# Optimization experiments

Measured on AMD Instinct MI355X. Metric: run time of the kernel, lower is better.

## Reference

```python
import jax, jax.numpy as jnp
import numpy as np


def _dct_mat(n):
    # Unnormalized DCT-II (torch_dct norm=None): X_k = 2 * sum_i x_i cos(pi*k*(2i+1)/(2n))
    idx = jnp.arange(n, dtype=jnp.float32)
    k = idx[:, None]
    i = idx[None, :]
    return 2.0 * jnp.cos(jnp.pi * k * (2.0 * i + 1.0) / (2.0 * n))  # [n_freq, n_pos]


def _idct_mat(n):
    # Exact inverse of _dct_mat: x_i = (1/n) * (X_0/2 + sum_{k>=1} X_k cos(pi*k*(2i+1)/(2n)))
    idx = jnp.arange(n, dtype=jnp.float32)
    i = idx[:, None]
    k = idx[None, :]
    w = jnp.where(jnp.arange(n) == 0, 0.5, 1.0) / n  # halve DC term
    return jnp.cos(jnp.pi * k * (2.0 * i + 1.0) / (2.0 * n)) * w[None, :]  # [n_pos, n_freq]


def _dct2(x, DH, DW):
    # separable 2D DCT-II over last two axes
    return jnp.einsum('nchw,kh,lw->nckl', x, DH, DW)


def _idct2(x, MH, MW):
    return jnp.einsum('nckl,hk,wl->nchw', x, MH, MW)


def setup_inputs() -> dict:
    key = jax.random.key(0)
    kx, kw = jax.random.split(key)
    x = jax.random.normal(kx, (64, 256, 32, 32), dtype=jnp.float32)
    # kaiming-uniform-like scale for a 256x3x3 fan-in
    weight = jax.random.normal(kw, (256, 256, 3, 3), dtype=jnp.float32) * 0.02
    return {"x": x, "weight": weight}


def reference(x, weight):
    N, C, H, W = x.shape
    F, _, HH, WW = weight.shape
    # pad filter on bottom/right to the full input spatial size
    kpad = jnp.pad(weight, ((0, 0), (0, 0), (0, H - HH), (0, W - WW)))
    DH, DW = _dct_mat(H), _dct_mat(W)
    MH, MW = _idct_mat(H), _idct_mat(W)
    X = _dct2(x, DH, DW)        # [N,C,H,W] frequency domain
    K = _dct2(kpad, DH, DW)     # [F,C,H,W] frequency domain
    # per-frequency channel contraction: matmul([N,C] x [C,F]) at every (h,w)
    R = jnp.einsum('nchw,fchw->nfhw', X, K)
    out = _idct2(R, MH, MW)
    out_H = H - HH + 1
    out_W = W - WW + 1
    return out[..., :out_H, :out_W]
```

## Files before the change

kernel.cpp:

```cpp
#include <hip/hip_runtime.h>
#include <hip/hip_bf16.h>

typedef __bf16 bf16x8 __attribute__((ext_vector_type(8)));
typedef float  f32x4  __attribute__((ext_vector_type(4)));
typedef unsigned short u16;
typedef u16 ushort8_t __attribute__((ext_vector_type(8)));

#define PI_D 3.14159265358979323846

__device__ __forceinline__ float rfl_f(float x){
  return __builtin_bit_cast(float, __builtin_amdgcn_readfirstlane(__builtin_bit_cast(int, x)));
}
__device__ __forceinline__ u16 bf16_bits(float f){
  __bf16 b = (__bf16)f;
  return __builtin_bit_cast(u16, b);
}
__device__ __forceinline__ float bf2f(u16 u){
  return __builtin_bit_cast(float, ((unsigned)u) << 16);
}

__global__ void k_init(float* __restrict__ Dm, float* __restrict__ Mm){
  for (int idx = threadIdx.x; idx < 1024; idx += 256){
    int r = idx >> 5, c = idx & 31;
    Dm[idx] = (float)(2.0 * cos(PI_D * (double)r * (double)(2*c+1) / 64.0));
    Mm[idx] = (float)(cos(PI_D * (double)c * (double)(2*r+1) / 64.0) * ((c==0)?0.5:1.0) / 32.0);
  }
}

__global__ __launch_bounds__(256) void k_wkb(const float* __restrict__ w,
                                             const float* __restrict__ Dm,
                                             u16* __restrict__ wkb){
  __shared__ float dks[32][3];
  int t = threadIdx.x;
  if (t < 96) dks[t/3][t%3] = Dm[(t/3)*32 + (t%3)];
  __syncthreads();
  int f = blockIdx.x, kf0 = blockIdx.y*4, c = t;
  const float* s = w + ((size_t)f*256 + c)*9;
  float wv9[9];
  #pragma unroll
  for (int j = 0; j < 9; ++j) wv9[j] = s[j];
  #pragma unroll
  for (int kq = 0; kq < 4; ++kq){
    int kf = kf0 + kq;
    float d0 = dks[kf][0], d1 = dks[kf][1], d2 = dks[kf][2];
    #pragma unroll
    for (int b = 0; b < 3; ++b){
      float v = d0*wv9[b] + d1*wv9[3+b] + d2*wv9[6+b];
      wkb[((size_t)(kf*3 + b) << 16) + (f << 8) + c] = bf16_bits(v);
    }
  }
}

__global__ __launch_bounds__(256) void k_dct2(const float* __restrict__ x,
                                              const float* __restrict__ Dm,
                                              u16* __restrict__ Xt){
  __shared__ __bf16 Dmb[32][40];
  __shared__ float  xl[4][32*37];
  __shared__ __bf16 t1[4][32*40];
  __shared__ u16    st[1024][20];
  int t = threadIdx.x;
  for (int idx = t; idx < 1024; idx += 256)
    Dmb[idx>>5][idx&31] = (__bf16)Dm[idx];
  __syncthreads();
  int wv = t >> 6, lane = t & 63, l4 = lane & 15, g = lane >> 4;
  bf16x8 dmf[2];
  dmf[0] = *(const bf16x8*)&Dmb[l4][g*8];
  dmf[1] = *(const bf16x8*)&Dmb[16+l4][g*8];
  int n = blockIdx.x, cb = blockIdx.y * 16;
  float* xw = xl[wv];
  __bf16* tw = t1[wv];
  f32x4 z = {0.f,0.f,0.f,0.f};
  for (int ci = 0; ci < 4; ++ci){
    int cl = wv*4 + ci;
    const float* xs = x + ((size_t)(n*256 + cb + cl)) * 1024;
    #pragma unroll
    for (int jr = 0; jr < 4; ++jr){
      int e = jr*256 + lane*4;
      float4 v = *(const float4*)(xs + e);
      float* p = xw + (e>>5)*37 + (e&31);
      p[0]=v.x; p[1]=v.y; p[2]=v.z; p[3]=v.w;
    }
    bf16x8 bf[2];
    #pragma unroll
    for (int nn = 0; nn < 2; ++nn){
      #pragma unroll
      for (int jj = 0; jj < 8; ++jj)
        bf[nn][jj] = (__bf16)xw[(g*8+jj)*37 + nn*16 + l4];
    }
    #pragma unroll
    for (int m = 0; m < 2; ++m){
      #pragma unroll
      for (int nn = 0; nn < 2; ++nn){
        f32x4 d = __builtin_amdgcn_mfma_f32_16x16x32_bf16(dmf[m], bf[nn], z, 0,0,0);
        #pragma unroll
        for (int r = 0; r < 4; ++r)
          tw[(m*16 + g*4 + r)*40 + nn*16 + l4] = (__bf16)d[r];
      }
    }
    bf16x8 a2[2];
    a2[0] = *(const bf16x8*)&tw[(l4)*40 + g*8];
    a2[1] = *(const bf16x8*)&tw[(16+l4)*40 + g*8];
    #pragma unroll
    for (int m2 = 0; m2 < 2; ++m2){
      #pragma unroll
      for (int nn2 = 0; nn2 < 2; ++nn2){
        f32x4 d = __builtin_amdgcn_mfma_f32_16x16x32_bf16(a2[m2], dmf[nn2], z, 0,0,0);
        #pragma unroll
        for (int r = 0; r < 4; ++r){
          int kk = m2*16 + g*4 + r, ll = nn2*16 + l4;
          st[kk*32 + ll][cl] = bf16_bits(d[r]);
        }
      }
    }
  }
  __syncthreads();
  #pragma unroll
  for (int rr = 0; rr < 8; ++rr){
    int kl = rr*128 + (t >> 1), half = t & 1;
    ushort4 v0 = *(const ushort4*)&st[kl][half*8];
    ushort4 v1 = *(const ushort4*)&st[kl][half*8 + 4];
    ushort8_t o;
    o[0]=v0.x; o[1]=v0.y; o[2]=v0.z; o[3]=v0.w;
    o[4]=v1.x; o[5]=v1.y; o[6]=v1.z; o[7]=v1.w;
    *(ushort8_t*)(Xt + (size_t)kl*16384 + (size_t)n*256 + cb + half*8) = o;
  }
}

__global__ __launch_bounds__(512) void k_mix(const u16* __restrict__ Xt,
                                             const u16* __restrict__ wkb,
                                             const float* __restrict__ Dm,
                                             u16* __restrict__ R){
  __shared__ __bf16 Bl[2][4][64][40];
  int t = threadIdx.x;
  int orig = blockIdx.x;
  int wid  = (orig & 7)*128 + (orig >> 3);
  int klg  = wid >> 2;
  int fb   = (wid & 3) * 64;
  int kl0 = klg * 4;
  int kf  = kl0 >> 5;
  int lb  = kl0 & 31;
  float dl[4][3];
  #pragma unroll
  for (int i = 0; i < 4; ++i){
    #pragma unroll
    for (int b = 0; b < 3; ++b) dl[i][b] = rfl_f(Dm[(lb+i)*32 + b]);
  }
  int lane = t & 63, wv = t >> 6;
  int kli = wv & 3, nh = wv >> 2;
  int l4 = lane & 15, g = lane >> 4;
  int rowi = t >> 3;
  int cq   = t & 7;
  f32x4 acc[2][4];
  #pragma unroll
  for (int m = 0; m < 2; ++m){
    #pragma unroll
    for (int nn = 0; nn < 4; ++nn){ f32x4 z={0.f,0.f,0.f,0.f}; acc[m][nn]=z; }
  }
  const u16* xb = Xt + (size_t)(kl0 + kli)*16384 + (size_t)(nh*32 + l4)*256 + g*8;
  const u16* wb = wkb + ((size_t)(kf*3) << 16) + ((fb + rowi) << 8) + cq*4;
  ushort4 wq[3];
  #pragma unroll
  for (int b = 0; b < 3; ++b) wq[b] = *(const ushort4*)(wb + ((size_t)b << 16));
  for (int cc = 0; cc < 8; ++cc){
    int p = cc & 1;
    bf16x8 afc[2];
    afc[0] = *(const bf16x8*)(xb + cc*32);
    afc[1] = *(const bf16x8*)(xb + cc*32 + 16*256);
    float tf[3][4];
    #pragma unroll
    for (int b = 0; b < 3; ++b){
      tf[b][0] = bf2f(wq[b].x); tf[b][1] = bf2f(wq[b].y);
      tf[b][2] = bf2f(wq[b].z); tf[b][3] = bf2f(wq[b].w);
    }
    if (cc < 7){
      const u16* wn = wb + (cc + 1)*32;
      #pragma unroll
      for (int b = 0; b < 3; ++b) wq[b] = *(const ushort4*)(wn + ((size_t)b << 16));
    }
    #pragma unroll
    for (int i = 0; i < 4; ++i){
      float s0 = dl[i][0]*tf[0][0] + dl[i][1]*tf[1][0] + dl[i][2]*tf[2][0];
      float s1 = dl[i][0]*tf[0][1] + dl[i][1]*tf[1][1] + dl[i][2]*tf[2][1];
      float s2 = dl[i][0]*tf[0][2] + dl[i][1]*tf[1][2] + dl[i][2]*tf[2][2];
      float s3 = dl[i][0]*tf[0][3] + dl[i][1]*tf[1][3] + dl[i][2]*tf[2][3];
      ushort4 pv;
      pv.x = bf16_bits(s0); pv.y = bf16_bits(s1);
      pv.z = bf16_bits(s2); pv.w = bf16_bits(s3);
      *(ushort4*)((u16*)&Bl[p][i][rowi][cq*4]) = pv;
    }
    __syncthreads();
    bf16x8 bfr[4];
    #pragma unroll
    for (int nn = 0; nn < 4; ++nn)
      bfr[nn] = *(const bf16x8*)&Bl[p][kli][nn*16 + l4][g*8];
    #pragma unroll
    for (int m = 0; m < 2; ++m){
      #pragma unroll
      for (int nn = 0; nn < 4; ++nn)
        acc[m][nn] = __builtin_amdgcn_mfma_f32_16x16x32_bf16(afc[m], bfr[nn], acc[m][nn], 0,0,0);
    }
  }
  int kl = kl0 + kli;
  #pragma unroll
  for (int m = 0; m < 2; ++m){
    #pragma unroll
    for (int nn = 0; nn < 4; ++nn){
      #pragma unroll
      for (int r = 0; r < 4; ++r){
        int n = nh*32 + m*16 + g*4 + r;
        R[((size_t)kl*64 + n)*256 + fb + nn*16 + l4] = bf16_bits(acc[m][nn][r]);
      }
    }
  }
}

__global__ __launch_bounds__(256) void k_idct2(const u16* __restrict__ R,
                                               const float* __restrict__ Mm,
                                               float* __restrict__ out){
  __shared__ __bf16 Mmb[32][40];
  __shared__ u16    st[1024][20];
  __shared__ __bf16 t2[4][32*40];
  int t = threadIdx.x;
  for (int idx = t; idx < 1024; idx += 256)
    Mmb[idx>>5][idx&31] = (__bf16)Mm[idx];
  int n = blockIdx.x, fbb = blockIdx.y * 16;
  #pragma unroll
  for (int rr = 0; rr < 8; ++rr){
    int kl = rr*128 + (t >> 1), half = t & 1;
    ushort8_t v = *(const ushort8_t*)(R + (size_t)kl*16384 + (size_t)n*256 + fbb + half*8);
    ushort4 a, b;
    a.x=v[0]; a.y=v[1]; a.z=v[2]; a.w=v[3];
    b.x=v[4]; b.y=v[5]; b.z=v[6]; b.w=v[7];
    *(ushort4*)&st[kl][half*8]     = a;
    *(ushort4*)&st[kl][half*8 + 4] = b;
  }
  __syncthreads();
  int wv = t>>6, lane = t&63, l4 = lane&15, g = lane>>4;
  bf16x8 mmf[2];
  mmf[0] = *(const bf16x8*)&Mmb[l4][g*8];
  mmf[1] = *(const bf16x8*)&Mmb[16+l4][g*8];
  f32x4 z = {0.f,0.f,0.f,0.f};
  __bf16* tw = t2[wv];
  for (int ci = 0; ci < 4; ++ci){
    int fl = wv*4 + ci;
    bf16x8 bfr[2];
    #pragma unroll
    for (int nn = 0; nn < 2; ++nn){
      #pragma unroll
      for (int jj = 0; jj < 8; ++jj)
        bfr[nn][jj] = __builtin_bit_cast(__bf16, st[(g*8+jj)*32 + nn*16 + l4][fl]);
    }
    #pragma unroll
    for (int m = 0; m < 2; ++m){
      #pragma unroll
      for (int nn = 0; nn < 2; ++nn){
        f32x4 d = __builtin_amdgcn_mfma_f32_16x16x32_bf16(mmf[m], bfr[nn], z, 0,0,0);
        #pragma unroll
        for (int r = 0; r < 4; ++r)
          tw[(m*16 + g*4 + r)*40 + nn*16 + l4] = (__bf16)d[r];
      }
    }
    bf16x8 a2[2];
    a2[0] = *(const bf16x8*)&tw[l4*40 + g*8];
    a2[1] = *(const bf16x8*)&tw[(16+l4)*40 + g*8];
    float* oo = out + (size_t)(n*256 + fbb + fl)*900;
    #pragma unroll
    for (int m2 = 0; m2 < 2; ++m2){
      #pragma unroll
      for (int nn2 = 0; nn2 < 2; ++nn2){
        f32x4 d = __builtin_amdgcn_mfma_f32_16x16x32_bf16(a2[m2], mmf[nn2], z, 0,0,0);
        #pragma unroll
        for (int r = 0; r < 4; ++r){
          int h = m2*16 + g*4 + r, w2 = nn2*16 + l4;
          if (h < 30 && w2 < 30) oo[h*30 + w2] = d[r];
        }
      }
    }
  }
}

extern "C" void kernel_launch(void* const* d_in, const int* in_sizes, int n_in,
                              void* d_out, int out_size, void* d_ws, size_t ws_size,
                              hipStream_t stream){
  (void)in_sizes; (void)n_in; (void)out_size; (void)ws_size;
  const float* x  = (const float*)d_in[0];
  const float* w  = (const float*)d_in[1];
  float* out = (float*)d_out;
  char* ws = (char*)d_ws;
  float* Dm = (float*)(ws + 0);
  float* Mm = (float*)(ws + 4096);
  u16* Xt   = (u16*)(ws + 8192);
  u16* R    = (u16*)(ws + 33562624);
  u16* wkb  = (u16*)(ws + 67117056);

  hipLaunchKernelGGL(k_init,  dim3(1),        dim3(256), 0, stream, Dm, Mm);
  hipLaunchKernelGGL(k_wkb,   dim3(256,8),    dim3(256), 0, stream, w, Dm, wkb);
  hipLaunchKernelGGL(k_dct2,  dim3(64,16),    dim3(256), 0, stream, x, Dm, Xt);
  hipLaunchKernelGGL(k_mix,   dim3(1024),     dim3(512), 0, stream, Xt, wkb, Dm, R);
  hipLaunchKernelGGL(k_idct2, dim3(64,16),    dim3(256), 0, stream, R, Mm, out);
}
```

Baseline: 83.36 us.

## Split forward DCT into natural-layout DCT plus separate LDS-tiled transpose kernel

The fused DCT kernel, which looped over channels and transposed through a large shared-memory staging buffer, is replaced by two kernels. A per-image DCT kernel writes results in natural [n,c,k,l] layout into a scratch region aliased with R, and a separate tiled transpose kernel rearranges them into the frequency-major layout consumed by the mixing kernel. This removes the big staging buffer and the per-block channel loop, which should raise occupancy. The cost is an extra 32 MB round trip through global memory and one more kernel launch.

```diff
diff --git a/kernel.cpp b/kernel.cpp
--- a/kernel.cpp
+++ b/kernel.cpp
@@ -51,13 +51,12 @@
   }
 }
 
-__global__ __launch_bounds__(256) void k_dct2(const float* __restrict__ x,
-                                              const float* __restrict__ Dm,
-                                              u16* __restrict__ Xt){
+__global__ __launch_bounds__(256) void k_dct(const float* __restrict__ x,
+                                             const float* __restrict__ Dm,
+                                             u16* __restrict__ Xnat){
   __shared__ __bf16 Dmb[32][40];
   __shared__ float  xl[4][32*37];
   __shared__ __bf16 t1[4][32*40];
-  __shared__ u16    st[1024][20];
   int t = threadIdx.x;
   for (int idx = t; idx < 1024; idx += 256)
     Dmb[idx>>5][idx&31] = (__bf16)Dm[idx];
@@ -66,63 +65,74 @@
   bf16x8 dmf[2];
   dmf[0] = *(const bf16x8*)&Dmb[l4][g*8];
   dmf[1] = *(const bf16x8*)&Dmb[16+l4][g*8];
-  int n = blockIdx.x, cb = blockIdx.y * 16;
+  int img = blockIdx.x*4 + wv;
+  const float* xs = x + (size_t)img*1024;
   float* xw = xl[wv];
+  #pragma unroll
+  for (int jr = 0; jr < 4; ++jr){
+    int e = jr*256 + lane*4;
+    float4 v = *(const float4*)(xs + e);
+    float* p = xw + (e>>5)*37 + (e&31);
+    p[0]=v.x; p[1]=v.y; p[2]=v.z; p[3]=v.w;
+  }
+  __syncthreads();
+  bf16x8 bf[2];
+  #pragma unroll
+  for (int nn = 0; nn < 2; ++nn){
+    #pragma unroll
+    for (int jj = 0; jj < 8; ++jj)
+      bf[nn][jj] = (__bf16)xw[(g*8+jj)*37 + nn*16 + l4];
+  }
+  f32x4 z = {0.f,0.f,0.f,0.f};
   __bf16* tw = t1[wv];
-  f32x4 z = {0.f,0.f,0.f,0.f};
-  for (int ci = 0; ci < 4; ++ci){
-    int cl = wv*4 + ci;
-    const float* xs = x + ((size_t)(n*256 + cb + cl)) * 1024;
-    #pragma unroll
-    for (int jr = 0; jr < 4; ++jr){
-      int e = jr*256 + lane*4;
-      float4 v = *(const float4*)(xs + e);
-      float* p = xw + (e>>5)*37 + (e&31);
-      p[0]=v.x; p[1]=v.y; p[2]=v.z; p[3]=v.w;
-    }
-    bf16x8 bf[2];
+  #pragma unroll
+  for (int m = 0; m < 2; ++m){
     #pragma unroll
     for (int nn = 0; nn < 2; ++nn){
-      #pragma unroll
-      for (int jj = 0; jj < 8; ++jj)
-        bf[nn][jj] = (__bf16)xw[(g*8+jj)*37 + nn*16 + l4];
-    }
-    #pragma unroll
-    for (int m = 0; m < 2; ++m){
-      #pragma unroll
-      for (int nn = 0; nn < 2; ++nn){
-        f32x4 d = __builtin_amdgcn_mfma_f32_16x16x32_bf16(dmf[m], bf[nn], z, 0,0,0);
-        #pragma unroll
-        for (int r = 0; r < 4; ++r)
-          tw[(m*16 + g*4 + r)*40 + nn*16 + l4] = (__bf16)d[r];
+      f32x4 d = __builtin_amdgcn_mfma_f32_16x16x32_bf16(dmf[m], bf[nn], z, 0,0,0);
+      #pragma unroll
+      for (int r = 0; r < 4; ++r)
+        tw[(m*16 + g*4 + r)*40 + nn*16 + l4] = (__bf16)d[r];
+    }
+  }
+  __syncthreads();
+  bf16x8 a2[2];
+  a2[0] = *(const bf16x8*)&tw[(l4)*40 + g*8];
+  a2[1] = *(const bf16x8*)&tw[(16+l4)*40 + g*8];
+  u16* xo = Xnat + (size_t)img*1024;
+  #pragma unroll
+  for (int m2 = 0; m2 < 2; ++m2){
+    #pragma unroll
+    for (int nn2 = 0; nn2 < 2; ++nn2){
+      f32x4 d = __builtin_amdgcn_mfma_f32_16x16x32_bf16(a2[m2], dmf[nn2], z, 0,0,0);
+      #pragma unroll
+      for (int r = 0; r < 4; ++r){
+        int kk = m2*16 + g*4 + r, ll = nn2*16 + l4;
+        xo[kk*32 + ll] = bf16_bits(d[r]);
       }
     }
-    bf16x8 a2[2];
-    a2[0] = *(const bf16x8*)&tw[(l4)*40 + g*8];
-    a2[1] = *(const bf16x8*)&tw[(16+l4)*40 + g*8];
-    #pragma unroll
-    for (int m2 = 0; m2 < 2; ++m2){
-      #pragma unroll
-      for (int nn2 = 0; nn2 < 2; ++nn2){
-        f32x4 d = __builtin_amdgcn_mfma_f32_16x16x32_bf16(a2[m2], dmf[nn2], z, 0,0,0);
-        #pragma unroll
-        for (int r = 0; r < 4; ++r){
-          int kk = m2*16 + g*4 + r, ll = nn2*16 + l4;
-          st[kk*32 + ll][cl] = bf16_bits(d[r]);
-        }
-      }
-    }
-  }
-  __syncthreads();
-  #pragma unroll
-  for (int rr = 0; rr < 8; ++rr){
-    int kl = rr*128 + (t >> 1), half = t & 1;
-    ushort4 v0 = *(const ushort4*)&st[kl][half*8];
-    ushort4 v1 = *(const ushort4*)&st[kl][half*8 + 4];
-    ushort8_t o;
-    o[0]=v0.x; o[1]=v0.y; o[2]=v0.z; o[3]=v0.w;
-    o[4]=v1.x; o[5]=v1.y; o[6]=v1.z; o[7]=v1.w;
-    *(ushort8_t*)(Xt + (size_t)kl*16384 + (size_t)n*256 + cb + half*8) = o;
+  }
+}
+
+__global__ __launch_bounds__(256) void k_tr(const u16* __restrict__ src,
+                                            u16* __restrict__ dst){
+  __shared__ u16 tile[64][66];
+  int klb = blockIdx.x*64, ncb = blockIdx.y*64;
+  int t = threadIdx.x, r0 = t >> 4, q = t & 15;
+  #pragma unroll
+  for (int jr = 0; jr < 4; ++jr){
+    int row = r0 + jr*16;
+    ushort4 v = *(const ushort4*)(src + (size_t)(ncb+row)*1024 + klb + q*4);
+    tile[row][q*4+0]=v.x; tile[row][q*4+1]=v.y; tile[row][q*4+2]=v.z; tile[row][q*4+3]=v.w;
+  }
+  __syncthreads();
+  #pragma unroll
+  for (int jr = 0; jr < 4; ++jr){
+    int kr = r0 + jr*16;
+    ushort4 o;
+    o.x = tile[q*4+0][kr]; o.y = tile[q*4+1][kr];
+    o.z = tile[q*4+2][kr]; o.w = tile[q*4+3][kr];
+    *(ushort4*)(dst + (size_t)(klb+kr)*16384 + ncb + q*4) = o;
   }
 }
 
@@ -290,12 +300,14 @@
   float* Dm = (float*)(ws + 0);
   float* Mm = (float*)(ws + 4096);
   u16* Xt   = (u16*)(ws + 8192);
+  u16* Xnat = (u16*)(ws + 33562624);
   u16* R    = (u16*)(ws + 33562624);
   u16* wkb  = (u16*)(ws + 67117056);
 
   hipLaunchKernelGGL(k_init,  dim3(1),        dim3(256), 0, stream, Dm, Mm);
   hipLaunchKernelGGL(k_wkb,   dim3(256,8),    dim3(256), 0, stream, w, Dm, wkb);
-  hipLaunchKernelGGL(k_dct2,  dim3(64,16),    dim3(256), 0, stream, x, Dm, Xt);
+  hipLaunchKernelGGL(k_dct,   dim3(4096),     dim3(256), 0, stream, x, Dm, Xnat);
+  hipLaunchKernelGGL(k_tr,    dim3(16,256),   dim3(256), 0, stream, Xnat, Xt);
   hipLaunchKernelGGL(k_mix,   dim3(1024),     dim3(512), 0, stream, Xt, wkb, Dm, R);
   hipLaunchKernelGGL(k_idct2, dim3(64,16),    dim3(256), 0, stream, R, Mm, out);
 }
```

Result: slower. 89.26 us (+7.1%).
